# Optimization experiments

Hardware: AMD Instinct MI355X
Metric: run time of the kernel (lower is better)

Reference implementation:

```python
import jax, jax.numpy as jnp
import numpy as np

PATCH = 3      # patch_size = (3, 3)
STRIDE = 1     # filter_patch_stride == compare_stride == 1
EPS = 1e-12    # F.normalize eps


def extract_patches(x, ph, pw, stride):
    """x: (B, C, H, W) -> (B, nH*nW, C, ph, pw), valid patches."""
    B, C, H, W = x.shape
    oh = (H - ph) // stride + 1
    ow = (W - pw) // stride + 1
    rows = (jnp.arange(oh) * stride)[:, None] + jnp.arange(ph)[None, :]  # (oh, ph)
    cols = (jnp.arange(ow) * stride)[:, None] + jnp.arange(pw)[None, :]  # (ow, pw)
    # gather -> (B, C, oh, ph, ow, pw)
    p = x[:, :, rows[:, :, None, None], cols[None, None, :, :]]
    return p.transpose(0, 2, 4, 1, 3, 5).reshape(B, oh * ow, C, ph, pw)


def l2norm(x, axis):
    # matches F.normalize(p=2): x / max(||x||, eps)
    return x / jnp.maximum(jnp.linalg.norm(x, axis=axis, keepdims=True), EPS)


def setup_inputs() -> dict:
    key = jax.random.key(0)
    k1, k2 = jax.random.split(key)
    pred_style = jax.random.normal(k1, (4, 256, 64, 64), dtype=jnp.float32)
    target_style = jax.random.normal(k2, (4, 256, 64, 64), dtype=jnp.float32)
    return {"pred_style": pred_style, "target_style": target_style}


def reference(pred_style, target_style):
    # patches of the raw (unnormalized) features
    tp = extract_patches(target_style, PATCH, PATCH, STRIDE)   # (B, nP, C, ph, pw)
    pp = extract_patches(pred_style, PATCH, PATCH, STRIDE)     # (B, nP, C, ph, pw)

    # best_match: normalize content feature over channels, style patches over channel dim (dim=2)
    x1n = l2norm(pred_style, axis=1)
    tpn = l2norm(tp, axis=2)
    x1p = extract_patches(x1n, PATCH, PATCH, STRIDE)           # (B, nP, C, ph, pw)

    # conv-as-cosine-correlation == batched patch dot products, then argmax over style patches
    scores = jnp.einsum('bqcij,bpcij->bqp', x1p, tpn)          # (B, nP, nP)
    match = jnp.argmax(scores, axis=2)                         # (B, nP)

    # gather best-matching target patches (indices detached in original via .data)
    new_t = jnp.take_along_axis(tp, match[:, :, None, None, None], axis=1)
    return jnp.mean((pp - new_t) ** 2)
```

## Files before the change

### kernel.cpp

```cpp
#include <hip/hip_runtime.h>
#include <hip/hip_bf16.h>

#define NB 4
#define CH 256
#define HH 64
#define WW 64
#define NPIX 4096
#define OH 62
#define NPATCH 3844
#define KDIM 256
#define EPSN 1e-12f
#define VROW 68

typedef __attribute__((ext_vector_type(8))) short short8;
typedef __attribute__((ext_vector_type(4))) float f32x4;

__device__ __forceinline__ float bf16_to_f32(unsigned short u) {
    return __uint_as_float((unsigned)u << 16);
}
__device__ __forceinline__ unsigned short f32_to_bf16(float f) {
    __hip_bfloat16 h = __float2bfloat16(f);
    return *(unsigned short*)&h;
}

__global__ __launch_bounds__(256) void k_prep(const float* __restrict__ pred,
                                              const float* __restrict__ tgt,
                                              __hip_bfloat16* __restrict__ Xn,
                                              __hip_bfloat16* __restrict__ Tn,
                                              float* __restrict__ ssP, float* __restrict__ invP,
                                              float* __restrict__ ssT, float* __restrict__ invT,
                                              unsigned long long* __restrict__ keys,
                                              float* __restrict__ out) {
    const int bz = blockIdx.y;
    const int b = bz >> 1, which = bz & 1;
    const float* src = (which ? tgt : pred) + (size_t)b * CH * NPIX;
    unsigned short* dst = (unsigned short*)((which ? Tn : Xn) + (size_t)b * NPIX * CH);
    float* ss_g  = (which ? ssT  : ssP)  + b * NPIX;
    float* inv_g = (which ? invT : invP) + b * NPIX;
    const int pix0 = blockIdx.x * 64;
    const int t = threadIdx.x, lane = t & 63, wv = t >> 6;

    int gid = (bz * 64 + blockIdx.x) * 256 + t;
    if (gid < NB * NPATCH) keys[gid] = 0ull;
    if (gid == 0) out[0] = 0.f;

    __shared__ unsigned short stage[CH][65];
    __shared__ float partial[4][64];
    __shared__ float inv_s[64];

    float ssacc = 0.f;
#pragma unroll 8
    for (int cc = 0; cc < 64; ++cc) {
        int c = wv * 64 + cc;
        float v = src[(size_t)c * NPIX + pix0 + lane];
        ssacc += v * v;
        stage[c][lane] = f32_to_bf16(v);
    }
    partial[wv][lane] = ssacc;
    __syncthreads();
    if (t < 64) {
        float ss = partial[0][t] + partial[1][t] + partial[2][t] + partial[3][t];
        float inv = 1.f / fmaxf(sqrtf(ss), EPSN);
        ss_g[pix0 + t] = ss;
        inv_g[pix0 + t] = inv;
        inv_s[t] = inv;
    }
    __syncthreads();
    for (int p = wv; p < 64; p += 4) {
        float iv = inv_s[p];
#pragma unroll
        for (int cb = 0; cb < 4; ++cb) {
            int c = cb * 64 + lane;
            float v = bf16_to_f32(stage[c][p]) * iv;
            dst[(size_t)(pix0 + p) * CH + c] = f32_to_bf16(v);
        }
    }
}

__device__ __forceinline__ void gload_lds16(const void* g, void* l) {
    __builtin_amdgcn_global_load_lds(
        (const __attribute__((address_space(1))) void*)g,
        (__attribute__((address_space(3))) void*)l, 16, 0, 0);
}

__global__ __launch_bounds__(256) void k_gemm(const __hip_bfloat16* __restrict__ A,
                                              const __hip_bfloat16* __restrict__ Bm,
                                              unsigned short* __restrict__ Dout) {
    __shared__ short As[128 * 32];
    __shared__ short Bs[128 * 32];
    const int z = blockIdx.z;
    const int t = threadIdx.x;
    const int lane = t & 63, wv = t >> 6;
    const int wm = wv >> 1, wn = wv & 1;
    const int row0 = blockIdx.y * 128, col0 = blockIdx.x * 128;
    const short* Ag = (const short*)A + (size_t)z * NPIX * CH;
    const short* Bg = (const short*)Bm + (size_t)z * NPIX * CH;
    unsigned short* D = Dout + (size_t)z * NPIX * NPIX;
    const int srow = t >> 2;
    const int kch  = (t & 3) * 8;

    f32x4 acc[4][4] = {};

    for (int k0 = 0; k0 < KDIM; k0 += 32) {
        gload_lds16(Ag + (size_t)(row0 + srow) * KDIM + k0 + kch,      As + wv * 512);
        gload_lds16(Ag + (size_t)(row0 + 64 + srow) * KDIM + k0 + kch, As + 2048 + wv * 512);
        gload_lds16(Bg + (size_t)(col0 + srow) * KDIM + k0 + kch,      Bs + wv * 512);
        gload_lds16(Bg + (size_t)(col0 + 64 + srow) * KDIM + k0 + kch, Bs + 2048 + wv * 512);
        __syncthreads();

        const int rsel = lane & 15, ksel = (lane >> 4) * 8;
        short8 a[4], bfr[4];
#pragma unroll
        for (int mi = 0; mi < 4; ++mi)
            a[mi] = *(const short8*)&As[(wm * 64 + mi * 16 + rsel) * 32 + ksel];
#pragma unroll
        for (int ni = 0; ni < 4; ++ni)
            bfr[ni] = *(const short8*)&Bs[(wn * 64 + ni * 16 + rsel) * 32 + ksel];
#pragma unroll
        for (int mi = 0; mi < 4; ++mi)
#pragma unroll
            for (int ni = 0; ni < 4; ++ni)
                acc[mi][ni] = __builtin_amdgcn_mfma_f32_16x16x32_bf16(a[mi], bfr[ni], acc[mi][ni], 0, 0, 0);
        __syncthreads();
    }
    const int rbase = (lane >> 4) * 4, cbase = lane & 15;
#pragma unroll
    for (int mi = 0; mi < 4; ++mi) {
#pragma unroll
        for (int ni = 0; ni < 4; ++ni) {
            int r0 = row0 + wm * 64 + mi * 16 + rbase;
            int c  = col0 + wn * 64 + ni * 16 + cbase;
#pragma unroll
            for (int r = 0; r < 4; ++r)
                D[(size_t)(r0 + r) * NPIX + c] = f32_to_bf16(acc[mi][ni][r]);
        }
    }
}

__device__ __forceinline__ void load_tile16(const unsigned short* __restrict__ D,
                                            int row, int col, float* f) {
    const unsigned short* rp = D + (size_t)row * NPIX + col;
    uint4 u0 = *(const uint4*)rp;
    uint4 u1 = *(const uint4*)(rp + 8);
    const unsigned* w0 = (const unsigned*)&u0;
    const unsigned* w1 = (const unsigned*)&u1;
#pragma unroll
    for (int w = 0; w < 4; ++w) {
        f[2 * w]         = bf16_to_f32((unsigned short)w0[w]);
        f[2 * w + 1]     = bf16_to_f32((unsigned short)(w0[w] >> 16));
        f[8 + 2 * w]     = bf16_to_f32((unsigned short)w1[w]);
        f[8 + 2 * w + 1] = bf16_to_f32((unsigned short)(w1[w] >> 16));
    }
}

__global__ __launch_bounds__(256) void k_score(const unsigned short* __restrict__ Dbase,
                                               unsigned long long* __restrict__ keys) {
    const int z = blockIdx.z;
    const unsigned short* D = Dbase + (size_t)z * NPIX * NPIX;
    const int pr = blockIdx.x, qr = blockIdx.y;
    const int t = threadIdx.x;

    __shared__ __align__(16) float V[64 * VROW];

    const int a = t >> 2, b0 = (t & 3) * 16;
    {
        float acc[16], f[16];
        load_tile16(D, (qr + 0) * 64 + a, (pr + 0) * 64 + b0, acc);
        load_tile16(D, (qr + 1) * 64 + a, (pr + 1) * 64 + b0, f);
#pragma unroll
        for (int e = 0; e < 16; ++e) acc[e] += f[e];
        load_tile16(D, (qr + 2) * 64 + a, (pr + 2) * 64 + b0, f);
#pragma unroll
        for (int e = 0; e < 16; ++e) acc[e] += f[e];
#pragma unroll
        for (int e = 0; e < 16; e += 4)
            *(f32x4*)&V[a * VROW + b0 + e] = *(const f32x4*)&acc[e];
    }
    __syncthreads();

    const int g = t >> 6, qc = t & 63;
    const int qcr = qc < OH ? qc : (OH - 1);
    const int pc0 = g * 16;
    const int kmax = (g == 3) ? 14 : 16;
    float r0[16], r1[20], r2[20];
#pragma unroll
    for (int e = 0; e < 16; e += 4)
        *(f32x4*)&r0[e] = *(const f32x4*)&V[qcr * VROW + pc0 + e];
#pragma unroll
    for (int e = 0; e < 20; e += 4)
        *(f32x4*)&r1[e] = *(const f32x4*)&V[(qcr + 1) * VROW + pc0 + e];
#pragma unroll
    for (int e = 0; e < 20; e += 4)
        *(f32x4*)&r2[e] = *(const f32x4*)&V[(qcr + 2) * VROW + pc0 + e];
    float best = -1e30f; int bpc = 0;
#pragma unroll
    for (int k = 0; k < 16; ++k) {
        float s = r0[k] + r1[k + 1] + r2[k + 2];
        if (k < kmax && s > best) { best = s; bpc = pc0 + k; }
    }
    if (qc < OH) {
        unsigned u = __float_as_uint(best);
        u = (best >= 0.f) ? (u | 0x80000000u) : ~u;
        unsigned long long key = ((unsigned long long)u << 12)
                               | (unsigned)((63 - pr) << 6) | (unsigned)(63 - bpc);
        atomicMax(&keys[(size_t)z * NPATCH + qr * OH + qc], key);
    }
}

__global__ void k_loss(const unsigned short* __restrict__ Dbase,
                       const unsigned long long* __restrict__ keys,
                       const float* __restrict__ ssPb, const float* __restrict__ invPb,
                       const float* __restrict__ ssTb, const float* __restrict__ invTb,
                       float* __restrict__ out) {
    const int z = blockIdx.y;
    const unsigned short* D = Dbase + (size_t)z * NPIX * NPIX;
    const float* ssP  = ssPb  + z * NPIX;
    const float* invP = invPb + z * NPIX;
    const float* ssT  = ssTb  + z * NPIX;
    const float* invT = invTb + z * NPIX;
    int q = blockIdx.x * 256 + threadIdx.x;
    float acc = 0.f;
    if (q < NPATCH) {
        int qr = q / OH, qc = q - qr * OH;
        int qpix = qr * WW + qc;
        unsigned long long key = keys[(size_t)z * NPATCH + q];
        int mpr = 63 - (int)((key >> 6) & 63);
        int mpc = 63 - (int)(key & 63);
        int mpix = mpr * WW + mpc;
#pragma unroll
        for (int i = 0; i < 3; ++i)
#pragma unroll
            for (int j = 0; j < 3; ++j) {
                int off = i * WW + j;
                int y = qpix + off, x = mpix + off;
                float Dv = bf16_to_f32(D[(size_t)y * NPIX + x]);
                float nP = ssP[y] * invP[y];
                float nT = ssT[x] * invT[x];
                acc += ssP[y] + ssT[x] - 2.f * Dv * nP * nT;
            }
    }
#pragma unroll
    for (int s = 32; s > 0; s >>= 1) acc += __shfl_down(acc, s, 64);
    if ((threadIdx.x & 63) == 0)
        atomicAdd(out, acc * (1.f / 35426304.f));
}

extern "C" void kernel_launch(void* const* d_in, const int* in_sizes, int n_in,
                              void* d_out, int out_size, void* d_ws, size_t ws_size,
                              hipStream_t stream) {
    const float* pred = (const float*)d_in[0];
    const float* tgt  = (const float*)d_in[1];
    char* ws = (char*)d_ws;
    unsigned short*     Dws  = (unsigned short*)(ws);
    __hip_bfloat16*     Xn   = (__hip_bfloat16*)(ws + 134217728);
    __hip_bfloat16*     Tn   = (__hip_bfloat16*)(ws + 142606336);
    float*              ssP  = (float*)(ws + 150994944);
    float*              invP = (float*)(ws + 151060480);
    float*              ssT  = (float*)(ws + 151126016);
    float*              invT = (float*)(ws + 151191552);
    unsigned long long* keys = (unsigned long long*)(ws + 151257088);

    k_prep<<<dim3(64, 8), 256, 0, stream>>>(pred, tgt, Xn, Tn, ssP, invP, ssT, invT,
                                            keys, (float*)d_out);
    k_gemm<<<dim3(32, 32, 4), 256, 0, stream>>>(Xn, Tn, Dws);
    k_score<<<dim3(62, 62, 4), 256, 0, stream>>>(Dws, keys);
    k_loss<<<dim3(16, 4), 256, 0, stream>>>(Dws, keys, ssP, invP, ssT, invT,
                                            (float*)d_out);
}
```

Before: 205.0 us.

## Walk score tiles along diagonals with a sliding window to reuse loads

```diff
diff --git a/kernel.cpp b/kernel.cpp
--- a/kernel.cpp
+++ b/kernel.cpp
@@ -11,6 +11,7 @@
 #define KDIM 256
 #define EPSN 1e-12f
 #define VROW 68
+#define SEG 16
 
 typedef __attribute__((ext_vector_type(8))) short short8;
 typedef __attribute__((ext_vector_type(4))) float f32x4;
@@ -155,55 +156,74 @@
 
 __global__ __launch_bounds__(256) void k_score(const unsigned short* __restrict__ Dbase,
                                                unsigned long long* __restrict__ keys) {
-    const int z = blockIdx.z;
+    const int z = blockIdx.y;
     const unsigned short* D = Dbase + (size_t)z * NPIX * NPIX;
-    const int pr = blockIdx.x, qr = blockIdx.y;
     const int t = threadIdx.x;
 
+    const int bx = blockIdx.x;
+    int d, s0;
+    if (bx < 108)      { int q = bx >> 2;  d = q - 13;  s0 = (bx & 3) * SEG; }
+    else if (bx < 204) { int r = bx - 108; int q = r / 3; int s = r - q * 3;
+                         d = (q < 16) ? (14 + q) : -(q - 2);  s0 = s * SEG; }
+    else if (bx < 268) { int r = bx - 204; int q = r >> 1;
+                         d = (q < 16) ? (30 + q) : -(q + 14);  s0 = (r & 1) * SEG; }
+    else               { int r = bx - 268;
+                         d = (r < 16) ? (46 + r) : -(r + 30);  s0 = 0; }
+    const int adg = d < 0 ? -d : d;
+    const int len = 62 - adg;
+    const int steps = min(SEG, len - s0);
+    const int qr0 = (d > 0 ? d : 0) + s0;
+    const int pr0 = qr0 - d;
+
     __shared__ __align__(16) float V[64 * VROW];
 
     const int a = t >> 2, b0 = (t & 3) * 16;
-    {
-        float acc[16], f[16];
-        load_tile16(D, (qr + 0) * 64 + a, (pr + 0) * 64 + b0, acc);
-        load_tile16(D, (qr + 1) * 64 + a, (pr + 1) * 64 + b0, f);
-#pragma unroll
-        for (int e = 0; e < 16; ++e) acc[e] += f[e];
-        load_tile16(D, (qr + 2) * 64 + a, (pr + 2) * 64 + b0, f);
-#pragma unroll
-        for (int e = 0; e < 16; ++e) acc[e] += f[e];
-#pragma unroll
-        for (int e = 0; e < 16; e += 4)
-            *(f32x4*)&V[a * VROW + b0 + e] = *(const f32x4*)&acc[e];
-    }
-    __syncthreads();
-
     const int g = t >> 6, qc = t & 63;
     const int qcr = qc < OH ? qc : (OH - 1);
     const int pc0 = g * 16;
     const int kmax = (g == 3) ? 14 : 16;
-    float r0[16], r1[20], r2[20];
-#pragma unroll
-    for (int e = 0; e < 16; e += 4)
-        *(f32x4*)&r0[e] = *(const f32x4*)&V[qcr * VROW + pc0 + e];
-#pragma unroll
-    for (int e = 0; e < 20; e += 4)
-        *(f32x4*)&r1[e] = *(const f32x4*)&V[(qcr + 1) * VROW + pc0 + e];
-#pragma unroll
-    for (int e = 0; e < 20; e += 4)
-        *(f32x4*)&r2[e] = *(const f32x4*)&V[(qcr + 2) * VROW + pc0 + e];
-    float best = -1e30f; int bpc = 0;
-#pragma unroll
-    for (int k = 0; k < 16; ++k) {
-        float s = r0[k] + r1[k + 1] + r2[k + 2];
-        if (k < kmax && s > best) { best = s; bpc = pc0 + k; }
-    }
-    if (qc < OH) {
-        unsigned u = __float_as_uint(best);
-        u = (best >= 0.f) ? (u | 0x80000000u) : ~u;
-        unsigned long long key = ((unsigned long long)u << 12)
-                               | (unsigned)((63 - pr) << 6) | (unsigned)(63 - bpc);
-        atomicMax(&keys[(size_t)z * NPATCH + qr * OH + qc], key);
+
+    float A[16], B[16], C[16];
+    load_tile16(D, (qr0 + 0) * 64 + a, (pr0 + 0) * 64 + b0, A);
+    load_tile16(D, (qr0 + 1) * 64 + a, (pr0 + 1) * 64 + b0, B);
+
+    for (int k = 0; k < steps; ++k) {
+        load_tile16(D, (qr0 + k + 2) * 64 + a, (pr0 + k + 2) * 64 + b0, C);
+        float v[16];
+#pragma unroll
+        for (int e = 0; e < 16; ++e) v[e] = A[e] + B[e] + C[e];
+        if (k) __syncthreads();
+#pragma unroll
+        for (int e = 0; e < 16; e += 4)
+            *(f32x4*)&V[a * VROW + b0 + e] = *(const f32x4*)&v[e];
+        __syncthreads();
+
+        float r0[16], r1[20], r2[20];
+#pragma unroll
+        for (int e = 0; e < 16; e += 4)
+            *(f32x4*)&r0[e] = *(const f32x4*)&V[qcr * VROW + pc0 + e];
+#pragma unroll
+        for (int e = 0; e < 20; e += 4)
+            *(f32x4*)&r1[e] = *(const f32x4*)&V[(qcr + 1) * VROW + pc0 + e];
+#pragma unroll
+        for (int e = 0; e < 20; e += 4)
+            *(f32x4*)&r2[e] = *(const f32x4*)&V[(qcr + 2) * VROW + pc0 + e];
+        float best = -1e30f; int bpc = 0;
+#pragma unroll
+        for (int kk = 0; kk < 16; ++kk) {
+            float s = r0[kk] + r1[kk + 1] + r2[kk + 2];
+            if (kk < kmax && s > best) { best = s; bpc = pc0 + kk; }
+        }
+        if (qc < OH) {
+            unsigned u = __float_as_uint(best);
+            u = (best >= 0.f) ? (u | 0x80000000u) : ~u;
+            unsigned long long key = ((unsigned long long)u << 12)
+                                   | (unsigned)((63 - (pr0 + k)) << 6)
+                                   | (unsigned)(63 - bpc);
+            atomicMax(&keys[(size_t)z * NPATCH + (qr0 + k) * OH + qc], key);
+        }
+#pragma unroll
+        for (int e = 0; e < 16; ++e) { A[e] = B[e]; B[e] = C[e]; }
     }
 }
 
@@ -263,7 +283,7 @@
     k_prep<<<dim3(64, 8), 256, 0, stream>>>(pred, tgt, Xn, Tn, ssP, invP, ssT, invT,
                                             keys, (float*)d_out);
     k_gemm<<<dim3(32, 32, 4), 256, 0, stream>>>(Xn, Tn, Dws);
-    k_score<<<dim3(62, 62, 4), 256, 0, stream>>>(Dws, keys);
+    k_score<<<dim3(300, 4), 256, 0, stream>>>(Dws, keys);
     k_loss<<<dim3(16, 4), 256, 0, stream>>>(Dws, keys, ssP, invP, ssT, invT,
                                             (float*)d_out);
 }
```

Result: faster. 188.1 us (-8.2%).
